# Kernel optimization log

Measured on AMD Instinct MI355X. Metric: run time of the kernel, lower is better.

Reference implementation:

```python
import jax, jax.numpy as jnp
import numpy as np

N_HEADS = 16

def setup_inputs() -> dict:
    key = jax.random.key(0)
    k1, k2 = jax.random.split(key)
    B, N, D = 2, 2048, 1024
    hidden_states = jax.random.normal(k1, (B, N, D), dtype=jnp.float32)
    # init std = initializer_range / sqrt(2 * num_layers * hidden_size)
    std = 0.02 / np.sqrt(2.0 * 24 * D)
    queries_weight = jax.random.normal(k2, (D, D), dtype=jnp.float32) * std
    return {"hidden_states": hidden_states, "queries_weight": queries_weight}

def reference(hidden_states, queries_weight):
    # DenseAttention, causal quadratic variant, multi-head, no relpe.
    B, N, D = hidden_states.shape
    H = N_HEADS
    hd = D // H
    # Q = X @ Wq, split into heads -> [B, H, N, hd]
    q = (hidden_states @ queries_weight).reshape(B, N, H, hd).transpose(0, 2, 1, 3)
    # K provided transposed per head -> [B, H, hd, N]; V -> [B, H, N, hd]
    xh = hidden_states.reshape(B, N, H, hd)
    k = xh.transpose(0, 2, 3, 1)
    v = xh.transpose(0, 2, 1, 3)
    # pre_attn = tril(Q @ K)  (no softmax in DenseAttention)
    pre_attn = jnp.tril(jnp.einsum('bhnd,bhdm->bhnm', q, k))  # [B,H,N,N]
    attn = jnp.einsum('bhnm,bhmd->bhnd', pre_attn, v)          # [B,H,N,hd]
    return attn.transpose(0, 2, 1, 3).reshape(B, N, D)
```

## Files before the change

### kernel.cpp

```cpp
#include <hip/hip_runtime.h>
#include <stdint.h>

#define Bz 2
#define Nseq 2048
#define Dm 1024
#define Hh 16
#define NCHUNK 32

typedef _Float16 half_t;
typedef __attribute__((ext_vector_type(8))) _Float16 h8v;
typedef __attribute__((ext_vector_type(4))) float f4v;

__global__ __launch_bounds__(256) void prep(const float* __restrict__ X,
                                            half_t* __restrict__ Xf,
                                            half_t* __restrict__ XT,
                                            float* __restrict__ U) {
  __shared__ half_t xt[64][72];
  __shared__ half_t xtT[64][72];
  int bx = blockIdx.x;
  int c = bx & 31, h = (bx >> 5) & 15, b = bx >> 9;
  int t = threadIdx.x;
  int r = t >> 2, c16 = (t & 3) * 16;

  {
    const float* src = X + ((size_t)b * Nseq + c * 64 + r) * Dm + h * 64 + c16;
    half_t* dXf = Xf + ((size_t)b * Nseq + c * 64 + r) * Dm + h * 64 + c16;
    h8v v0, v1;
#pragma unroll
    for (int j = 0; j < 8; j++) { v0[j] = (half_t)src[j]; v1[j] = (half_t)src[8 + j]; }
    *(h8v*)&xt[r][c16] = v0;
    *(h8v*)&xt[r][c16 + 8] = v1;
    *(h8v*)&dXf[0] = v0;
    *(h8v*)&dXf[8] = v1;
  }
  __syncthreads();
  {
    int d = r, mg = c16;
    h8v v0, v1;
#pragma unroll
    for (int j = 0; j < 8; j++) { v0[j] = xt[mg + j][d]; v1[j] = xt[mg + 8 + j][d]; }
    *(h8v*)&xtT[d][mg] = v0;
    *(h8v*)&xtT[d][mg + 8] = v1;
    half_t* dXT = XT + ((size_t)(b * Hh + h) * 64 + d) * Nseq + c * 64 + mg;
    *(h8v*)&dXT[0] = v0;
    *(h8v*)&dXT[8] = v1;
  }
  __syncthreads();
  int wave = t >> 6, lane = t & 63;
  int lrow = lane & 15, lk = (lane >> 4) * 8;
  h8v a0 = *(h8v*)&xtT[wave * 16 + lrow][lk];
  h8v a1 = *(h8v*)&xtT[wave * 16 + lrow][32 + lk];
  f4v acc[4] = {};
#pragma unroll
  for (int j = 0; j < 4; j++) {
    acc[j] = __builtin_amdgcn_mfma_f32_16x16x32_f16(a0, *(h8v*)&xtT[j * 16 + lrow][lk], acc[j], 0, 0, 0);
    acc[j] = __builtin_amdgcn_mfma_f32_16x16x32_f16(a1, *(h8v*)&xtT[j * 16 + lrow][32 + lk], acc[j], 0, 0, 0);
  }
  float* ub = U + (size_t)bx * 4096;
#pragma unroll
  for (int j = 0; j < 4; j++)
#pragma unroll
    for (int v = 0; v < 4; v++)
      ub[(size_t)(wave * 16 + (lane >> 4) * 4 + v) * 64 + j * 16 + (lane & 15)] = acc[j][v];
}

__global__ __launch_bounds__(256) void prep_w(const float* __restrict__ w,
                                              half_t* __restrict__ WT) {
  __shared__ float tile[64][65];
  int tk = blockIdx.x >> 4, tn = blockIdx.x & 15;
  int t = threadIdx.x;
  int r = t >> 2, c0 = (t & 3) * 16;
  const float* src = w + (size_t)(tk * 64 + r) * Dm + tn * 64 + c0;
#pragma unroll
  for (int j = 0; j < 16; j++) tile[r][c0 + j] = src[j];
  __syncthreads();
  half_t* dst = WT + (size_t)(tn * 64 + r) * Dm + tk * 64 + c0;
  h8v v0, v1;
#pragma unroll
  for (int j = 0; j < 8; j++) {
    v0[j] = (half_t)(tile[c0 + j][r] * 4096.0f);
    v1[j] = (half_t)(tile[c0 + 8 + j][r] * 4096.0f);
  }
  *(h8v*)&dst[0] = v0;
  *(h8v*)&dst[8] = v1;
}

#define KP 40
__global__ __launch_bounds__(256) void qgemm16(const half_t* __restrict__ A,
                                               const half_t* __restrict__ Bw,
                                               half_t* __restrict__ Qs) {
  __shared__ half_t sA[128][KP], sB[128][KP];
  int bm = blockIdx.x >> 3, bn = blockIdx.x & 7;
  int t = threadIdx.x;
  int wave = t >> 6, lane = t & 63;
  int wr = wave >> 1, wc = wave & 1;
  int lrow = lane & 15, lk = (lane >> 4) * 8;
  f4v acc[4][4] = {};

  int srow = t >> 1, skc = (t & 1) * 16;
  const half_t* pA = A + (size_t)(bm * 128 + srow) * Dm + skc;
  const half_t* pB = Bw + (size_t)(bn * 128 + srow) * Dm + skc;

  for (int k0 = 0; k0 < Dm; k0 += 32) {
    *(h8v*)&sA[srow][skc]     = *(const h8v*)(pA + k0);
    *(h8v*)&sA[srow][skc + 8] = *(const h8v*)(pA + k0 + 8);
    *(h8v*)&sB[srow][skc]     = *(const h8v*)(pB + k0);
    *(h8v*)&sB[srow][skc + 8] = *(const h8v*)(pB + k0 + 8);
    __syncthreads();
    h8v af[4], bf[4];
#pragma unroll
    for (int i = 0; i < 4; i++) {
      af[i] = *(h8v*)&sA[wr * 64 + i * 16 + lrow][lk];
      bf[i] = *(h8v*)&sB[wc * 64 + i * 16 + lrow][lk];
    }
#pragma unroll
    for (int i = 0; i < 4; i++)
#pragma unroll
      for (int j = 0; j < 4; j++)
        acc[i][j] = __builtin_amdgcn_mfma_f32_16x16x32_f16(af[i], bf[j], acc[i][j], 0, 0, 0);
    __syncthreads();
  }
#pragma unroll
  for (int i = 0; i < 4; i++)
#pragma unroll
    for (int j = 0; j < 4; j++) {
      int row = bm * 128 + wr * 64 + i * 16 + (lane >> 4) * 4;
      int col = bn * 128 + wc * 64 + j * 16 + (lane & 15);
#pragma unroll
      for (int v = 0; v < 4; v++)
        Qs[(size_t)(row + v) * Dm + col] = (half_t)(acc[i][j][v] * 0.0625f);
    }
}

__global__ __launch_bounds__(256) void prefix16(const float* __restrict__ U,
                                                half_t* __restrict__ S16) {
  int g = blockIdx.x * 256 + threadIdx.x;
  int bh = g >> 12, e = g & 4095;
  float run = 0.f;
  for (int c = 0; c < NCHUNK; c++) {
    size_t idx = ((size_t)bh * NCHUNK + c) * 4096 + e;
    S16[idx] = (half_t)run;
    run += U[idx];
  }
}

__global__ __launch_bounds__(256) void attn16(const half_t* __restrict__ Xf,
                                              const half_t* __restrict__ XT,
                                              const half_t* __restrict__ Qs,
                                              const half_t* __restrict__ S16,
                                              float* __restrict__ out) {
  __shared__ half_t qs[64][72];
  __shared__ half_t ks[64][72];
  __shared__ half_t vts[64][72];
  __shared__ half_t ss[64][72];
  __shared__ half_t pt[64][72];
  int bx = blockIdx.x;
  int c = bx & 31, h = (bx >> 5) & 15, b = bx >> 9;
  int t = threadIdx.x;
  int r = t >> 2, c16 = (t & 3) * 16;
  {
    size_t rowoff = ((size_t)b * Nseq + c * 64 + r) * Dm + h * 64 + c16;
    *(h8v*)&qs[r][c16]     = *(const h8v*)(Qs + rowoff);
    *(h8v*)&qs[r][c16 + 8] = *(const h8v*)(Qs + rowoff + 8);
    *(h8v*)&ks[r][c16]     = *(const h8v*)(Xf + rowoff);
    *(h8v*)&ks[r][c16 + 8] = *(const h8v*)(Xf + rowoff + 8);
    size_t toff = ((size_t)(b * Hh + h) * 64 + r) * Nseq + c * 64 + c16;
    *(h8v*)&vts[r][c16]     = *(const h8v*)(XT + toff);
    *(h8v*)&vts[r][c16 + 8] = *(const h8v*)(XT + toff + 8);
    size_t soff = ((size_t)(b * Hh + h) * NCHUNK + c) * 4096 + r * 64 + c16;
    *(h8v*)&ss[r][c16]     = *(const h8v*)(S16 + soff);
    *(h8v*)&ss[r][c16 + 8] = *(const h8v*)(S16 + soff + 8);
  }
  __syncthreads();
  int wave = t >> 6, lane = t & 63;
  int lrow = lane & 15, lk = (lane >> 4) * 8;
  h8v aq0 = *(h8v*)&qs[wave * 16 + lrow][lk];
  h8v aq1 = *(h8v*)&qs[wave * 16 + lrow][32 + lk];
  f4v p[4] = {};
#pragma unroll
  for (int j = 0; j < 4; j++) {
    p[j] = __builtin_amdgcn_mfma_f32_16x16x32_f16(aq0, *(h8v*)&ks[j * 16 + lrow][lk], p[j], 0, 0, 0);
    p[j] = __builtin_amdgcn_mfma_f32_16x16x32_f16(aq1, *(h8v*)&ks[j * 16 + lrow][32 + lk], p[j], 0, 0, 0);
  }
  int orow = wave * 16 + (lane >> 4) * 4;
#pragma unroll
  for (int j = 0; j < 4; j++)
#pragma unroll
    for (int v = 0; v < 4; v++) {
      int rr = orow + v, mm = j * 16 + (lane & 15);
      pt[rr][mm] = (half_t)((mm <= rr) ? p[j][v] : 0.f);
    }
  __syncthreads();
  h8v ap0 = *(h8v*)&pt[wave * 16 + lrow][lk];
  h8v ap1 = *(h8v*)&pt[wave * 16 + lrow][32 + lk];
  f4v o[4] = {};
#pragma unroll
  for (int j = 0; j < 4; j++) {
    o[j] = __builtin_amdgcn_mfma_f32_16x16x32_f16(ap0, *(h8v*)&vts[j * 16 + lrow][lk], o[j], 0, 0, 0);
    o[j] = __builtin_amdgcn_mfma_f32_16x16x32_f16(ap1, *(h8v*)&vts[j * 16 + lrow][32 + lk], o[j], 0, 0, 0);
    o[j] = __builtin_amdgcn_mfma_f32_16x16x32_f16(aq0, *(h8v*)&ss[j * 16 + lrow][lk], o[j], 0, 0, 0);
    o[j] = __builtin_amdgcn_mfma_f32_16x16x32_f16(aq1, *(h8v*)&ss[j * 16 + lrow][32 + lk], o[j], 0, 0, 0);
  }
  float* dst = out + ((size_t)b * Nseq + c * 64) * Dm + h * 64;
#pragma unroll
  for (int j = 0; j < 4; j++)
#pragma unroll
    for (int v = 0; v < 4; v++)
      dst[(size_t)(orow + v) * Dm + j * 16 + (lane & 15)] = o[j][v] * 0.00390625f;
}

extern "C" void kernel_launch(void* const* d_in, const int* in_sizes, int n_in,
                              void* d_out, int out_size, void* d_ws, size_t ws_size,
                              hipStream_t stream) {
  const float* X = (const float*)d_in[0];
  const float* W = (const float*)d_in[1];
  float* out = (float*)d_out;

  float* U = (float*)d_ws;
  half_t* Xf = (half_t*)(U + 4194304);
  half_t* XT = Xf + 4194304;
  half_t* Qs = XT + 4194304;
  half_t* S16 = Qs + 4194304;
  half_t* WT = S16 + 4194304;

  prep<<<1024, 256, 0, stream>>>(X, Xf, XT, U);
  prep_w<<<256, 256, 0, stream>>>(W, WT);
  qgemm16<<<256, 256, 0, stream>>>(Xf, WT, Qs);
  prefix16<<<512, 256, 0, stream>>>(U, S16);
  attn16<<<1024, 256, 0, stream>>>(Xf, XT, Qs, S16, out);
}
```

Measured before the change: 119.8 us.

## Fuse prep kernels, drop XT buffer, swizzled LDS-direct GEMM, vectorize prefix

Merges the X and W preparation kernels into one launch and stops writing a transposed copy of X to global memory; the attention kernel now transposes the K tile in shared memory to build V^T. The Q GEMM switches to BK=64 with direct global-to-LDS loads into an XOR-swizzled layout, which avoids bank conflicts. The prefix-sum kernel processes four elements per thread with float4 loads. Together these cut a launch and global traffic, at the cost of an extra LDS transpose inside attn16 and one larger unpadded LDS tile in the GEMM.

After: 108.1 us. 9.8% less time.

```diff
diff --git a/kernel.cpp b/kernel.cpp
--- a/kernel.cpp
+++ b/kernel.cpp
@@ -6,118 +6,133 @@
 #define Dm 1024
 #define Hh 16
 #define NCHUNK 32
+#define BK 64
 
 typedef _Float16 half_t;
 typedef __attribute__((ext_vector_type(8))) _Float16 h8v;
+typedef __attribute__((ext_vector_type(4))) _Float16 h4v;
 typedef __attribute__((ext_vector_type(4))) float f4v;
 
-__global__ __launch_bounds__(256) void prep(const float* __restrict__ X,
-                                            half_t* __restrict__ Xf,
-                                            half_t* __restrict__ XT,
-                                            float* __restrict__ U) {
-  __shared__ half_t xt[64][72];
-  __shared__ half_t xtT[64][72];
+#define GLDS(g, l)                                                        \
+  __builtin_amdgcn_global_load_lds(                                       \
+      (const __attribute__((address_space(1))) void*)(g),                 \
+      (__attribute__((address_space(3))) void*)(l), 16, 0, 0)
+
+__global__ __launch_bounds__(256) void prep_fused(const float* __restrict__ X,
+                                                  const float* __restrict__ W,
+                                                  half_t* __restrict__ Xf,
+                                                  float* __restrict__ U,
+                                                  half_t* __restrict__ WT) {
+  __shared__ double smem_[2304];
   int bx = blockIdx.x;
-  int c = bx & 31, h = (bx >> 5) & 15, b = bx >> 9;
   int t = threadIdx.x;
-  int r = t >> 2, c16 = (t & 3) * 16;
-
-  {
-    const float* src = X + ((size_t)b * Nseq + c * 64 + r) * Dm + h * 64 + c16;
-    half_t* dXf = Xf + ((size_t)b * Nseq + c * 64 + r) * Dm + h * 64 + c16;
+  if (bx < 1024) {
+    half_t(*xt)[72] = (half_t(*)[72])smem_;
+    half_t(*xtT)[72] = (half_t(*)[72])(smem_ + 1152);
+    int c = bx & 31, h = (bx >> 5) & 15, b = bx >> 9;
+    int r = t >> 2, c16 = (t & 3) * 16;
+    {
+      const float* src = X + ((size_t)b * Nseq + c * 64 + r) * Dm + h * 64 + c16;
+      half_t* dXf = Xf + ((size_t)b * Nseq + c * 64 + r) * Dm + h * 64 + c16;
+      h8v v0, v1;
+#pragma unroll
+      for (int j = 0; j < 8; j++) { v0[j] = (half_t)src[j]; v1[j] = (half_t)src[8 + j]; }
+      *(h8v*)&xt[r][c16] = v0;
+      *(h8v*)&xt[r][c16 + 8] = v1;
+      *(h8v*)&dXf[0] = v0;
+      *(h8v*)&dXf[8] = v1;
+    }
+    __syncthreads();
+    {
+      int d = r, mg = c16;
+      h8v v0, v1;
+#pragma unroll
+      for (int j = 0; j < 8; j++) { v0[j] = xt[mg + j][d]; v1[j] = xt[mg + 8 + j][d]; }
+      *(h8v*)&xtT[d][mg] = v0;
+      *(h8v*)&xtT[d][mg + 8] = v1;
+    }
+    __syncthreads();
+    int wave = t >> 6, lane = t & 63;
+    int lrow = lane & 15, lk = (lane >> 4) * 8;
+    h8v a0 = *(h8v*)&xtT[wave * 16 + lrow][lk];
+    h8v a1 = *(h8v*)&xtT[wave * 16 + lrow][32 + lk];
+    f4v acc[4] = {};
+#pragma unroll
+    for (int j = 0; j < 4; j++) {
+      acc[j] = __builtin_amdgcn_mfma_f32_16x16x32_f16(a0, *(h8v*)&xtT[j * 16 + lrow][lk], acc[j], 0, 0, 0);
+      acc[j] = __builtin_amdgcn_mfma_f32_16x16x32_f16(a1, *(h8v*)&xtT[j * 16 + lrow][32 + lk], acc[j], 0, 0, 0);
+    }
+    float* ub = U + (size_t)bx * 4096;
+#pragma unroll
+    for (int j = 0; j < 4; j++)
+#pragma unroll
+      for (int v = 0; v < 4; v++)
+        ub[(size_t)(wave * 16 + (lane >> 4) * 4 + v) * 64 + j * 16 + (lane & 15)] = acc[j][v];
+  } else {
+    float(*tile)[65] = (float(*)[65])smem_;
+    int bw = bx - 1024;
+    int tk = bw >> 4, tn = bw & 15;
+    int r = t >> 2, c0 = (t & 3) * 16;
+    const float* src = W + (size_t)(tk * 64 + r) * Dm + tn * 64 + c0;
+#pragma unroll
+    for (int j = 0; j < 16; j++) tile[r][c0 + j] = src[j];
+    __syncthreads();
+    half_t* dst = WT + (size_t)(tn * 64 + r) * Dm + tk * 64 + c0;
     h8v v0, v1;
 #pragma unroll
-    for (int j = 0; j < 8; j++) { v0[j] = (half_t)src[j]; v1[j] = (half_t)src[8 + j]; }
-    *(h8v*)&xt[r][c16] = v0;
-    *(h8v*)&xt[r][c16 + 8] = v1;
-    *(h8v*)&dXf[0] = v0;
-    *(h8v*)&dXf[8] = v1;
-  }
-  __syncthreads();
-  {
-    int d = r, mg = c16;
-    h8v v0, v1;
-#pragma unroll
-    for (int j = 0; j < 8; j++) { v0[j] = xt[mg + j][d]; v1[j] = xt[mg + 8 + j][d]; }
-    *(h8v*)&xtT[d][mg] = v0;
-    *(h8v*)&xtT[d][mg + 8] = v1;
-    half_t* dXT = XT + ((size_t)(b * Hh + h) * 64 + d) * Nseq + c * 64 + mg;
-    *(h8v*)&dXT[0] = v0;
-    *(h8v*)&dXT[8] = v1;
-  }
-  __syncthreads();
-  int wave = t >> 6, lane = t & 63;
-  int lrow = lane & 15, lk = (lane >> 4) * 8;
-  h8v a0 = *(h8v*)&xtT[wave * 16 + lrow][lk];
-  h8v a1 = *(h8v*)&xtT[wave * 16 + lrow][32 + lk];
-  f4v acc[4] = {};
-#pragma unroll
-  for (int j = 0; j < 4; j++) {
-    acc[j] = __builtin_amdgcn_mfma_f32_16x16x32_f16(a0, *(h8v*)&xtT[j * 16 + lrow][lk], acc[j], 0, 0, 0);
-    acc[j] = __builtin_amdgcn_mfma_f32_16x16x32_f16(a1, *(h8v*)&xtT[j * 16 + lrow][32 + lk], acc[j], 0, 0, 0);
-  }
-  float* ub = U + (size_t)bx * 4096;
-#pragma unroll
-  for (int j = 0; j < 4; j++)
-#pragma unroll
-    for (int v = 0; v < 4; v++)
-      ub[(size_t)(wave * 16 + (lane >> 4) * 4 + v) * 64 + j * 16 + (lane & 15)] = acc[j][v];
-}
-
-__global__ __launch_bounds__(256) void prep_w(const float* __restrict__ w,
-                                              half_t* __restrict__ WT) {
-  __shared__ float tile[64][65];
-  int tk = blockIdx.x >> 4, tn = blockIdx.x & 15;
-  int t = threadIdx.x;
-  int r = t >> 2, c0 = (t & 3) * 16;
-  const float* src = w + (size_t)(tk * 64 + r) * Dm + tn * 64 + c0;
-#pragma unroll
-  for (int j = 0; j < 16; j++) tile[r][c0 + j] = src[j];
-  __syncthreads();
-  half_t* dst = WT + (size_t)(tn * 64 + r) * Dm + tk * 64 + c0;
-  h8v v0, v1;
-#pragma unroll
-  for (int j = 0; j < 8; j++) {
-    v0[j] = (half_t)(tile[c0 + j][r] * 4096.0f);
-    v1[j] = (half_t)(tile[c0 + 8 + j][r] * 4096.0f);
-  }
-  *(h8v*)&dst[0] = v0;
-  *(h8v*)&dst[8] = v1;
-}
-
-#define KP 40
+    for (int j = 0; j < 8; j++) {
+      v0[j] = (half_t)(tile[c0 + j][r] * 4096.0f);
+      v1[j] = (half_t)(tile[c0 + 8 + j][r] * 4096.0f);
+    }
+    *(h8v*)&dst[0] = v0;
+    *(h8v*)&dst[8] = v1;
+  }
+}
+
 __global__ __launch_bounds__(256) void qgemm16(const half_t* __restrict__ A,
                                                const half_t* __restrict__ Bw,
                                                half_t* __restrict__ Qs) {
-  __shared__ half_t sA[128][KP], sB[128][KP];
+  __shared__ half_t sA[128 * BK];
+  __shared__ half_t sB[128 * BK];
   int bm = blockIdx.x >> 3, bn = blockIdx.x & 7;
   int t = threadIdx.x;
   int wave = t >> 6, lane = t & 63;
   int wr = wave >> 1, wc = wave & 1;
-  int lrow = lane & 15, lk = (lane >> 4) * 8;
+  int lrow = lane & 15, g4 = lane >> 4;
+
+  int srow = wave * 32 + (lane >> 3);
+  int scol = ((lane & 7) ^ (lane >> 3)) * 8;
+  const half_t* pA = A + (size_t)(bm * 128 + srow) * Dm + scol;
+  const half_t* pB = Bw + (size_t)(bn * 128 + srow) * Dm + scol;
+  half_t* ldsA = sA + (size_t)(wave * 32) * BK;
+  half_t* ldsB = sB + (size_t)(wave * 32) * BK;
+
   f4v acc[4][4] = {};
-
-  int srow = t >> 1, skc = (t & 1) * 16;
-  const half_t* pA = A + (size_t)(bm * 128 + srow) * Dm + skc;
-  const half_t* pB = Bw + (size_t)(bn * 128 + srow) * Dm + skc;
-
-  for (int k0 = 0; k0 < Dm; k0 += 32) {
-    *(h8v*)&sA[srow][skc]     = *(const h8v*)(pA + k0);
-    *(h8v*)&sA[srow][skc + 8] = *(const h8v*)(pA + k0 + 8);
-    *(h8v*)&sB[srow][skc]     = *(const h8v*)(pB + k0);
-    *(h8v*)&sB[srow][skc + 8] = *(const h8v*)(pB + k0 + 8);
-    __syncthreads();
-    h8v af[4], bf[4];
-#pragma unroll
-    for (int i = 0; i < 4; i++) {
-      af[i] = *(h8v*)&sA[wr * 64 + i * 16 + lrow][lk];
-      bf[i] = *(h8v*)&sB[wc * 64 + i * 16 + lrow][lk];
-    }
-#pragma unroll
-    for (int i = 0; i < 4; i++)
-#pragma unroll
-      for (int j = 0; j < 4; j++)
-        acc[i][j] = __builtin_amdgcn_mfma_f32_16x16x32_f16(af[i], bf[j], acc[i][j], 0, 0, 0);
+  for (int k0 = 0; k0 < Dm; k0 += BK) {
+#pragma unroll
+    for (int q = 0; q < 4; q++) {
+      GLDS(pA + (size_t)q * 8 * Dm + k0, ldsA + q * 8 * BK);
+      GLDS(pB + (size_t)q * 8 * Dm + k0, ldsB + q * 8 * BK);
+    }
+    __syncthreads();
+#pragma unroll
+    for (int ks = 0; ks < 2; ks++) {
+      h8v af[4], bf[4];
+#pragma unroll
+      for (int i = 0; i < 4; i++) {
+        int rowA = wr * 64 + i * 16 + lrow;
+        uint offA = (uint)rowA * 128 + (((uint)(ks * 64 + g4 * 16)) ^ (uint)((rowA & 7) << 4));
+        af[i] = *(const h8v*)((const char*)sA + offA);
+        int rowB = wc * 64 + i * 16 + lrow;
+        uint offB = (uint)rowB * 128 + (((uint)(ks * 64 + g4 * 16)) ^ (uint)((rowB & 7) << 4));
+        bf[i] = *(const h8v*)((const char*)sB + offB);
+      }
+#pragma unroll
+      for (int i = 0; i < 4; i++)
+#pragma unroll
+        for (int j = 0; j < 4; j++)
+          acc[i][j] = __builtin_amdgcn_mfma_f32_16x16x32_f16(af[i], bf[j], acc[i][j], 0, 0, 0);
+    }
     __syncthreads();
   }
 #pragma unroll
@@ -135,17 +150,21 @@
 __global__ __launch_bounds__(256) void prefix16(const float* __restrict__ U,
                                                 half_t* __restrict__ S16) {
   int g = blockIdx.x * 256 + threadIdx.x;
-  int bh = g >> 12, e = g & 4095;
-  float run = 0.f;
+  int bh = g >> 10, e4 = g & 1023;
+  const float4* u = (const float4*)(U + (size_t)bh * NCHUNK * 4096) + e4;
+  half_t* s = S16 + (size_t)bh * NCHUNK * 4096 + e4 * 4;
+  float4 run = {0.f, 0.f, 0.f, 0.f};
   for (int c = 0; c < NCHUNK; c++) {
-    size_t idx = ((size_t)bh * NCHUNK + c) * 4096 + e;
-    S16[idx] = (half_t)run;
-    run += U[idx];
+    h4v sv;
+    sv[0] = (half_t)run.x; sv[1] = (half_t)run.y;
+    sv[2] = (half_t)run.z; sv[3] = (half_t)run.w;
+    *(h4v*)(s + (size_t)c * 4096) = sv;
+    float4 uv = u[(size_t)c * 1024];
+    run.x += uv.x; run.y += uv.y; run.z += uv.z; run.w += uv.w;
   }
 }
 
 __global__ __launch_bounds__(256) void attn16(const half_t* __restrict__ Xf,
-                                              const half_t* __restrict__ XT,
                                               const half_t* __restrict__ Qs,
                                               const half_t* __restrict__ S16,
                                               float* __restrict__ out) {
@@ -164,9 +183,6 @@
     *(h8v*)&qs[r][c16 + 8] = *(const h8v*)(Qs + rowoff + 8);
     *(h8v*)&ks[r][c16]     = *(const h8v*)(Xf + rowoff);
     *(h8v*)&ks[r][c16 + 8] = *(const h8v*)(Xf + rowoff + 8);
-    size_t toff = ((size_t)(b * Hh + h) * 64 + r) * Nseq + c * 64 + c16;
-    *(h8v*)&vts[r][c16]     = *(const h8v*)(XT + toff);
-    *(h8v*)&vts[r][c16 + 8] = *(const h8v*)(XT + toff + 8);
     size_t soff = ((size_t)(b * Hh + h) * NCHUNK + c) * 4096 + r * 64 + c16;
     *(h8v*)&ss[r][c16]     = *(const h8v*)(S16 + soff);
     *(h8v*)&ss[r][c16 + 8] = *(const h8v*)(S16 + soff + 8);
@@ -182,6 +198,14 @@
     p[j] = __builtin_amdgcn_mfma_f32_16x16x32_f16(aq0, *(h8v*)&ks[j * 16 + lrow][lk], p[j], 0, 0, 0);
     p[j] = __builtin_amdgcn_mfma_f32_16x16x32_f16(aq1, *(h8v*)&ks[j * 16 + lrow][32 + lk], p[j], 0, 0, 0);
   }
+  {
+    int d = r, mg = c16;
+    h8v v0, v1;
+#pragma unroll
+    for (int j = 0; j < 8; j++) { v0[j] = ks[mg + j][d]; v1[j] = ks[mg + 8 + j][d]; }
+    *(h8v*)&vts[d][mg] = v0;
+    *(h8v*)&vts[d][mg + 8] = v1;
+  }
   int orow = wave * 16 + (lane >> 4) * 4;
 #pragma unroll
   for (int j = 0; j < 4; j++)
@@ -218,14 +242,12 @@
 
   float* U = (float*)d_ws;
   half_t* Xf = (half_t*)(U + 4194304);
-  half_t* XT = Xf + 4194304;
-  half_t* Qs = XT + 4194304;
+  half_t* Qs = Xf + 4194304;
   half_t* S16 = Qs + 4194304;
   half_t* WT = S16 + 4194304;
 
-  prep<<<1024, 256, 0, stream>>>(X, Xf, XT, U);
-  prep_w<<<256, 256, 0, stream>>>(W, WT);
+  prep_fused<<<1280, 256, 0, stream>>>(X, W, Xf, U, WT);
   qgemm16<<<256, 256, 0, stream>>>(Xf, WT, Qs);
-  prefix16<<<512, 256, 0, stream>>>(U, S16);
-  attn16<<<1024, 256, 0, stream>>>(Xf, XT, Qs, S16, out);
-}
+  prefix16<<<128, 256, 0, stream>>>(U, S16);
+  attn16<<<1024, 256, 0, stream>>>(Xf, Qs, S16, out);
+}
```
